# Performance work log

Measured on AMD Instinct MI355X. Metric: run time of the kernel, lower is better.

Reference implementation:

```python
import jax, jax.numpy as jnp
import numpy as np

BETA = 2.0  # init kwarg


def setup_inputs() -> dict:
    key = jax.random.key(0)
    k1, k2, k3 = jax.random.split(key, 3)
    B, T, V = 64, 188, 32000
    # scores must be positive (they are fed to log); uniform in (1e-4, 1)
    targets_scores = jax.random.uniform(k1, (B, T, V), jnp.float32, minval=1e-4, maxval=1.0)
    targets_ground_truth = jax.random.randint(k2, (B, T), 0, V).astype(jnp.int64)
    lengths = jax.random.randint(k3, (B,), 1, T + 1).astype(jnp.int64)
    return {
        "targets_scores": targets_scores,
        "targets_ground_truth": targets_ground_truth,
        "lengths": lengths,
    }


def reference(targets_scores, targets_ground_truth, lengths):
    B, T, V = targets_scores.shape
    # validity mask from lengths (the hand-built length_matrix)
    mask = (jnp.arange(T)[None, :] < lengths[:, None]).astype(targets_scores.dtype)  # [B,T]
    # gather score of the ground-truth class at each position
    gathered = jnp.take_along_axis(
        targets_scores, targets_ground_truth[..., None], axis=2
    )[..., 0]  # [B,T]
    # per-element beta weighting: weight 1 when gt==0, else beta
    weight = jnp.where(targets_ground_truth == 0, 1.0, BETA).astype(targets_scores.dtype)
    loss = -(mask * weight * jnp.log(gathered)).sum() / B
    return loss.reshape(1)
```

## Files before the change

### kernel.cpp

```cpp
#include <hip/hip_runtime.h>
#include <hip/hip_bf16.h>


#define BETA 2.0f

__global__ void loss_partial_kernel(const float* __restrict__ scores,
                                    const int* __restrict__ gt,
                                    const int* __restrict__ lengths,
                                    float* __restrict__ partials,
                                    int BT, int T, int V) {
    int idx = blockIdx.x * blockDim.x + threadIdx.x;
    float val = 0.0f;
    if (idx < BT) {
        int b = idx / T;
        int t = idx - b * T;
        if (t < lengths[b]) {
            int g = gt[idx];
            float s = scores[(size_t)idx * (size_t)V + (size_t)g];
            float w = (g == 0) ? 1.0f : BETA;
            val = w * logf(s);
        }
    }
    #pragma unroll
    for (int off = 32; off > 0; off >>= 1)
        val += __shfl_down(val, off, 64);

    __shared__ float sm[2];
    int lane = threadIdx.x & 63;
    int wid  = threadIdx.x >> 6;
    if (lane == 0) sm[wid] = val;
    __syncthreads();
    if (threadIdx.x == 0) partials[blockIdx.x] = sm[0] + sm[1];
}

__global__ void loss_final_kernel(const float* __restrict__ partials,
                                  float* __restrict__ out,
                                  int n, float invB) {
    float val = 0.0f;
    for (int i = threadIdx.x; i < n; i += 64)
        val += partials[i];
    #pragma unroll
    for (int off = 32; off > 0; off >>= 1)
        val += __shfl_down(val, off, 64);
    if (threadIdx.x == 0)
        out[0] = -val * invB;
}

extern "C" void kernel_launch(void* const* d_in, const int* in_sizes, int n_in,
                              void* d_out, int out_size, void* d_ws, size_t ws_size,
                              hipStream_t stream) {
    const float* scores  = (const float*)d_in[0];
    const int*   gt      = (const int*)d_in[1];
    const int*   lengths = (const int*)d_in[2];
    float* out = (float*)d_out;
    float* ws  = (float*)d_ws;

    int BT = in_sizes[1];
    int B  = in_sizes[2];
    int T  = BT / B;
    int V  = (int)((long long)in_sizes[0] / (long long)BT);

    const int BLOCK = 128;
    int blocks = (BT + BLOCK - 1) / BLOCK;

    loss_partial_kernel<<<blocks, BLOCK, 0, stream>>>(scores, gt, lengths, ws, BT, T, V);
    loss_final_kernel<<<1, 64, 0, stream>>>(ws, out, blocks, 1.0f / (float)B);
}
```

Baseline: 11.44 us.

## Fuse partial and final reduction into one cooperative kernel with grid sync

Replaces the two-kernel reduction with a single cooperative launch of up to 64 blocks of 1024 threads. Each thread accumulates over a grid-stride loop, blocks reduce hierarchically into workspace, and a grid-wide sync lets block 0 produce the final scalar. This removes the second kernel launch and its gap, at the cost of grid-sync overhead and fewer, larger blocks for the scattered gather loads.

Measured after the change: 29.30 us. +156.1%, slower.

```diff
diff --git a/kernel.cpp b/kernel.cpp
--- a/kernel.cpp
+++ b/kernel.cpp
@@ -1,49 +1,58 @@
 #include <hip/hip_runtime.h>
 #include <hip/hip_bf16.h>
+#include <hip/hip_cooperative_groups.h>
+
+namespace cg = cooperative_groups;
 
 
 #define BETA 2.0f
+#define NTHR 1024
 
-__global__ void loss_partial_kernel(const float* __restrict__ scores,
-                                    const int* __restrict__ gt,
-                                    const int* __restrict__ lengths,
-                                    float* __restrict__ partials,
-                                    int BT, int T, int V) {
-    int idx = blockIdx.x * blockDim.x + threadIdx.x;
+__global__ void loss_fused_kernel(const float* __restrict__ scores,
+                                  const int* __restrict__ gt,
+                                  const int* __restrict__ lengths,
+                                  float* __restrict__ out,
+                                  float* __restrict__ ws,
+                                  int BT, int T, int V, float invB) {
     float val = 0.0f;
-    if (idx < BT) {
+    for (int idx = blockIdx.x * blockDim.x + threadIdx.x; idx < BT;
+         idx += gridDim.x * blockDim.x) {
         int b = idx / T;
         int t = idx - b * T;
         if (t < lengths[b]) {
             int g = gt[idx];
             float s = scores[(size_t)idx * (size_t)V + (size_t)g];
             float w = (g == 0) ? 1.0f : BETA;
-            val = w * logf(s);
+            val += w * logf(s);
         }
     }
+
     #pragma unroll
     for (int off = 32; off > 0; off >>= 1)
         val += __shfl_down(val, off, 64);
 
-    __shared__ float sm[2];
+    __shared__ float sm[NTHR / 64];
     int lane = threadIdx.x & 63;
     int wid  = threadIdx.x >> 6;
     if (lane == 0) sm[wid] = val;
     __syncthreads();
-    if (threadIdx.x == 0) partials[blockIdx.x] = sm[0] + sm[1];
-}
+    if (wid == 0) {
+        float v = (lane < NTHR / 64) ? sm[lane] : 0.0f;
+        #pragma unroll
+        for (int off = 32; off > 0; off >>= 1)
+            v += __shfl_down(v, off, 64);
+        if (lane == 0) ws[blockIdx.x] = v;
+    }
 
-__global__ void loss_final_kernel(const float* __restrict__ partials,
-                                  float* __restrict__ out,
-                                  int n, float invB) {
-    float val = 0.0f;
-    for (int i = threadIdx.x; i < n; i += 64)
-        val += partials[i];
-    #pragma unroll
-    for (int off = 32; off > 0; off >>= 1)
-        val += __shfl_down(val, off, 64);
-    if (threadIdx.x == 0)
-        out[0] = -val * invB;
+    cg::this_grid().sync();
+
+    if (blockIdx.x == 0 && wid == 0) {
+        float v = (lane < (int)gridDim.x) ? ws[lane] : 0.0f;
+        #pragma unroll
+        for (int off = 32; off > 0; off >>= 1)
+            v += __shfl_down(v, off, 64);
+        if (lane == 0) out[0] = -v * invB;
+    }
 }
 
 extern "C" void kernel_launch(void* const* d_in, const int* in_sizes, int n_in,
@@ -59,10 +68,14 @@
     int B  = in_sizes[2];
     int T  = BT / B;
     int V  = (int)((long long)in_sizes[0] / (long long)BT);
+    float invB = 1.0f / (float)B;
 
-    const int BLOCK = 128;
-    int blocks = (BT + BLOCK - 1) / BLOCK;
+    int blocks = (BT + NTHR - 1) / NTHR;
+    if (blocks > 64) blocks = 64;
 
-    loss_partial_kernel<<<blocks, BLOCK, 0, stream>>>(scores, gt, lengths, ws, BT, T, V);
-    loss_final_kernel<<<1, 64, 0, stream>>>(ws, out, blocks, 1.0f / (float)B);
+    void* args[] = { (void*)&scores, (void*)&gt, (void*)&lengths,
+                     (void*)&out, (void*)&ws,
+                     (void*)&BT, (void*)&T, (void*)&V, (void*)&invB };
+    hipLaunchCooperativeKernel((const void*)loss_fused_kernel,
+                               dim3(blocks), dim3(NTHR), args, 0, stream);
 }
```

## Fuse partial and final reduction into one kernel with flag-based grid sync

Applied to the files above, without the earlier changes.

Merges the two-kernel reduction into a single launch. Each block publishes its partial sum and then sets a magic flag with release semantics. Block 0 spin-waits on all the flags, reduces the partials and writes the output, then resets the flags for the next call. This removes the second kernel launch and its gap, at the cost of block 0 spinning, which relies on every block being resident or eventually scheduled. It also assumes nblk <= 128 (BT=12032 gives 94 blocks), that the workspace is at least 512 bytes plus the flag array, and that the flags start out not equal to the magic value.

Measured after the change: 9.551 us. -16.5%, faster.

```diff
diff --git a/kernel.cpp b/kernel.cpp
--- a/kernel.cpp
+++ b/kernel.cpp
@@ -2,14 +2,22 @@
 #include <hip/hip_bf16.h>
 
 
-#define BETA 2.0f
+#define BETA  2.0f
+#define NTHR  128
+#define MAGIC 0x5EEDF00DCAFEBEEFULL
 
-__global__ void loss_partial_kernel(const float* __restrict__ scores,
+__global__ void loss_onepass_kernel(const float* __restrict__ scores,
                                     const int* __restrict__ gt,
                                     const int* __restrict__ lengths,
+                                    float* __restrict__ out,
                                     float* __restrict__ partials,
-                                    int BT, int T, int V) {
-    int idx = blockIdx.x * blockDim.x + threadIdx.x;
+                                    unsigned long long* __restrict__ flags,
+                                    int BT, int T, int V, float invB, int nblk) {
+    const int tid  = threadIdx.x;
+    const int lane = tid & 63;
+    const int wid  = tid >> 6;
+
+    int idx = blockIdx.x * NTHR + tid;
     float val = 0.0f;
     if (idx < BT) {
         int b = idx / T;
@@ -17,33 +25,47 @@
         if (t < lengths[b]) {
             int g = gt[idx];
             float s = scores[(size_t)idx * (size_t)V + (size_t)g];
-            float w = (g == 0) ? 1.0f : BETA;
-            val = w * logf(s);
+            val = ((g == 0) ? 1.0f : BETA) * logf(s);
         }
     }
     #pragma unroll
     for (int off = 32; off > 0; off >>= 1)
         val += __shfl_down(val, off, 64);
 
-    __shared__ float sm[2];
-    int lane = threadIdx.x & 63;
-    int wid  = threadIdx.x >> 6;
+    __shared__ float sm[NTHR / 64];
     if (lane == 0) sm[wid] = val;
     __syncthreads();
-    if (threadIdx.x == 0) partials[blockIdx.x] = sm[0] + sm[1];
-}
+    if (tid == 0) {
+        float p = sm[0] + sm[1];
+        __hip_atomic_store(&partials[blockIdx.x], p,
+                           __ATOMIC_RELAXED, __HIP_MEMORY_SCOPE_AGENT);
+        __hip_atomic_store(&flags[blockIdx.x], MAGIC,
+                           __ATOMIC_RELEASE, __HIP_MEMORY_SCOPE_AGENT);
+    }
 
-__global__ void loss_final_kernel(const float* __restrict__ partials,
-                                  float* __restrict__ out,
-                                  int n, float invB) {
-    float val = 0.0f;
-    for (int i = threadIdx.x; i < n; i += 64)
-        val += partials[i];
+    if (blockIdx.x != 0) return;
+
+    if (tid < nblk) {
+        while (__hip_atomic_load(&flags[tid], __ATOMIC_ACQUIRE,
+                                 __HIP_MEMORY_SCOPE_AGENT) != MAGIC) {
+            __builtin_amdgcn_s_sleep(1);
+        }
+    }
+    float v = (tid < nblk)
+        ? __hip_atomic_load(&partials[tid], __ATOMIC_RELAXED,
+                            __HIP_MEMORY_SCOPE_AGENT)
+        : 0.0f;
     #pragma unroll
     for (int off = 32; off > 0; off >>= 1)
-        val += __shfl_down(val, off, 64);
-    if (threadIdx.x == 0)
-        out[0] = -val * invB;
+        v += __shfl_down(v, off, 64);
+    __syncthreads();
+    if (lane == 0) sm[wid] = v;
+    __syncthreads();
+    if (tid == 0) out[0] = -(sm[0] + sm[1]) * invB;
+
+    if (tid < nblk)
+        __hip_atomic_store(&flags[tid], 0ULL,
+                           __ATOMIC_RELEASE, __HIP_MEMORY_SCOPE_AGENT);
 }
 
 extern "C" void kernel_launch(void* const* d_in, const int* in_sizes, int n_in,
@@ -53,16 +75,19 @@
     const int*   gt      = (const int*)d_in[1];
     const int*   lengths = (const int*)d_in[2];
     float* out = (float*)d_out;
-    float* ws  = (float*)d_ws;
 
     int BT = in_sizes[1];
     int B  = in_sizes[2];
     int T  = BT / B;
     int V  = (int)((long long)in_sizes[0] / (long long)BT);
+    float invB = 1.0f / (float)B;
 
-    const int BLOCK = 128;
-    int blocks = (BT + BLOCK - 1) / BLOCK;
+    int nblk = (BT + NTHR - 1) / NTHR;
 
-    loss_partial_kernel<<<blocks, BLOCK, 0, stream>>>(scores, gt, lengths, ws, BT, T, V);
-    loss_final_kernel<<<1, 64, 0, stream>>>(ws, out, blocks, 1.0f / (float)B);
+    float* partials = (float*)d_ws;
+    unsigned long long* flags =
+        (unsigned long long*)((char*)d_ws + 512);
+
+    loss_onepass_kernel<<<nblk, NTHR, 0, stream>>>(
+        scores, gt, lengths, out, partials, flags, BT, T, V, invB, nblk);
 }
```
